# Kernel tuning notes

Measured on AMD Instinct MI355X. Metric: run time of the kernel, lower is better.

## Reference

```python
import jax, jax.numpy as jnp
import numpy as np

B, L, D = 1, 2048, 1024
H, F, HD = 16, 16, 64  # heads, feature_dim, head_dim
EPS = 1e-12


def setup_inputs() -> dict:
    key = jax.random.key(0)
    k1, k2, k3, k4, k5 = jax.random.split(key, 5)
    s = lambda fan_in: 1.0 / np.sqrt(fan_in)
    return {
        "hidden_states": jax.random.normal(k1, (B, L, D), jnp.float32),
        "Wq": jax.random.normal(k2, (D, H * F), jnp.float32) * s(D),
        "Wk": jax.random.normal(k3, (D, H * F), jnp.float32) * s(D),
        "Wv": jax.random.normal(k4, (D, H * HD), jnp.float32) * s(D),
        "Wo": jax.random.normal(k5, (H * HD, D), jnp.float32) * s(H * HD),
    }


def reference(hidden_states, Wq, Wk, Wv, Wo):
    b, l, _ = hidden_states.shape
    # projections (nn.Linear, no bias); reshape to (b, h, l, d)
    q = (hidden_states @ Wq).reshape(b, l, H, F).transpose(0, 2, 1, 3)
    k = (hidden_states @ Wk).reshape(b, l, H, F).transpose(0, 2, 1, 3)
    v = (hidden_states @ Wv).reshape(b, l, H, HD).transpose(0, 2, 1, 3)
    # feature map is identity. Causal quadratic linear attention:
    A = jnp.einsum("bhnd,bhmd->bhnm", q, k)          # [b,h,l,l]
    A = jnp.tril(A)
    y = jnp.einsum("bhnm,bhme->bhne", A, v)          # [b,h,l,hd]
    # denominator: q . cumsum(k)
    z = 1.0 / (jnp.einsum("bhld,bhld->bhl", q, jnp.cumsum(k, axis=2)) + EPS)
    y = y * z[..., None]
    # merge heads and output projection
    y = y.transpose(0, 2, 1, 3).reshape(b, l, H * HD)
    return y @ Wo
```

## Files before the change

### kernel.cpp

```cpp
#include <hip/hip_runtime.h>

constexpr int L  = 2048;
constexpr int D  = 1024;
constexpr int H  = 16;
constexpr int F  = 16;
constexpr int HD = 64;
constexpr int CHUNK = 128;
constexpr int NC = L / CHUNK;

typedef __bf16 bf16x8 __attribute__((ext_vector_type(8)));
typedef float  f32x16 __attribute__((ext_vector_type(16)));
typedef int    i32x4  __attribute__((ext_vector_type(4)));

__device__ __forceinline__ ushort f2bf(float f) {
  uint u = __builtin_bit_cast(uint, f);
  uint r = (u + 0x7FFFu + ((u >> 16) & 1u)) >> 16;
  return (ushort)r;
}

__device__ __forceinline__ void split5(float x, signed char s[5]) {
  float t = rintf(x * 16.f);              s[0] = (signed char)t;
  float r = fmaf(t, -6.25e-2f, x);
  t = rintf(r * 2048.f);                  s[1] = (signed char)t;
  r = fmaf(t, -4.8828125e-4f, r);
  t = rintf(r * 262144.f);                s[2] = (signed char)t;
  r = fmaf(t, -3.814697265625e-6f, r);
  t = rintf(r * 33554432.f);              s[3] = (signed char)t;
  r = fmaf(t, -2.9802322387695312e-8f, r);
  t = rintf(r * 4294967296.f);            s[4] = (signed char)t;
}

__global__ __launch_bounds__(256) void prep_all(
    const float* __restrict__ X,
    const float* __restrict__ Wv, const float* __restrict__ Wo,
    const float* __restrict__ Wq, const float* __restrict__ Wk,
    ushort* __restrict__ Ah, signed char* __restrict__ A8,
    ushort* __restrict__ BvT, ushort* __restrict__ BoT, signed char* __restrict__ W8) {
  __shared__ float t[32][33];
  const int tid = threadIdx.x;
  const int b = blockIdx.x;
  if (b < 2048) {
    const int plane = L * D;
    int idx = b * 256 + tid;
    float4 v = ((const float4*)X)[idx];
    ushort4 hh;
    hh.x = f2bf(v.x); hh.y = f2bf(v.y); hh.z = f2bf(v.z); hh.w = f2bf(v.w);
    ((ushort4*)Ah)[idx] = hh;
    signed char sx[5], sy[5], sz[5], sw[5];
    split5(v.x, sx); split5(v.y, sy); split5(v.z, sz); split5(v.w, sw);
    #pragma unroll
    for (int s = 0; s < 5; ++s) {
      char4 c; c.x = sx[s]; c.y = sy[s]; c.z = sz[s]; c.w = sw[s];
      ((char4*)(A8 + (size_t)s * plane))[idx] = c;
    }
    return;
  }
  const int bb = b - 2048;
  const int z = bb >> 10;
  const int bx = (bb & 1023) & 31, by = (bb & 1023) >> 5;
  const int lx = tid & 31, ly = tid >> 5;
  if (z == 2) {
    if (bx >= 16) return;
    const int plane = 512 * 1024;
    const int bn = bx * 32, bk = by * 32;
    const float* W = (bn < 256) ? Wq : Wk;
    const int wn = bn & 255;
    #pragma unroll
    for (int i = 0; i < 32; i += 8)
      t[ly + i][lx] = W[(size_t)(bk + ly + i) * 256 + wn + lx];
    __syncthreads();
    #pragma unroll
    for (int i = 0; i < 32; i += 8) {
      float v = t[lx][ly + i];
      signed char s[5];
      split5(v, s);
      size_t base = (size_t)(bn + ly + i) * 1024 + bk + lx;
      #pragma unroll
      for (int si = 0; si < 5; ++si) W8[(size_t)si * plane + base] = s[si];
    }
    return;
  }
  const float* W = z ? Wo : Wv;
  ushort* BT = z ? BoT : BvT;
  const int bn = bx * 32, bk = by * 32;
  #pragma unroll
  for (int i = 0; i < 32; i += 8)
    t[ly + i][lx] = W[(size_t)(bk + ly + i) * 1024 + bn + lx];
  __syncthreads();
  #pragma unroll
  for (int i = 0; i < 32; i += 8) {
    float v = t[lx][ly + i];
    BT[(size_t)(bn + ly + i) * 1024 + bk + lx] = f2bf(v);
  }
}

__global__ __launch_bounds__(512) void gemm_v_qk(
    const signed char* __restrict__ A8, const signed char* __restrict__ W8,
    float* __restrict__ Qo, float* __restrict__ Ko,
    const ushort* __restrict__ Av, const ushort* __restrict__ BvT,
    float* __restrict__ Vb) {
  __shared__ __align__(16) char lds_raw[51200];
  const int tid = threadIdx.x;
  const int bid = blockIdx.x;
  const int wave = tid >> 6, lane = tid & 63;

  if (bid < 256) {
    auto As = (signed char (*)[64][80])(lds_raw);
    auto Bs = (signed char (*)[64][80])(lds_raw + 25600);
    const int aplane = L * D;
    const int bplane = 512 * 1024;
    const int wm = (wave >> 2) * 32;
    const int wn = (wave & 3) * 16;
    int b2 = (bid & 7) * 32 + (bid >> 3);
    const int brow = (b2 >> 3) * 64, bcol = (b2 & 7) * 64;
    const int fr = lane & 15, kq = (lane >> 4) * 16;

    i32x4 acc[2][5];
    #pragma unroll
    for (int fm = 0; fm < 2; ++fm)
      #pragma unroll
      for (int g = 0; g < 5; ++g)
        #pragma unroll
        for (int r = 0; r < 4; ++r) acc[fm][g][r] = 0;

    for (int k0 = 0; k0 < D; k0 += 64) {
      #pragma unroll
      for (int i = 0; i < 5; ++i) {
        int c = i * 512 + tid;
        int side = (c >= 1280);
        int cc = side ? c - 1280 : c;
        int slice = cc >> 8, row = (cc & 255) >> 2, c16 = (cc & 3) * 16;
        const signed char* src = side
            ? &W8[(size_t)slice * bplane + (size_t)(bcol + row) * 1024 + k0 + c16]
            : &A8[(size_t)slice * aplane + (size_t)(brow + row) * 1024 + k0 + c16];
        int4 val = *(const int4*)src;
        signed char* dst = side ? &Bs[slice][row][c16] : &As[slice][row][c16];
        *(int4*)dst = val;
      }
      __syncthreads();
      i32x4 bfr[5], afr[2][5];
      #pragma unroll
      for (int s = 0; s < 5; ++s) bfr[s] = *(const i32x4*)&Bs[s][wn + fr][kq];
      #pragma unroll
      for (int fm = 0; fm < 2; ++fm)
        #pragma unroll
        for (int s = 0; s < 5; ++s)
          afr[fm][s] = *(const i32x4*)&As[s][wm + fm * 16 + fr][kq];
      #pragma unroll
      for (int fm = 0; fm < 2; ++fm) {
        acc[fm][0] = __builtin_amdgcn_mfma_i32_16x16x64_i8(afr[fm][0], bfr[0], acc[fm][0], 0, 0, 0);
        #pragma unroll
        for (int g = 1; g < 5; ++g)
          #pragma unroll
          for (int i = 0; i <= g; ++i)
            acc[fm][g] = __builtin_amdgcn_mfma_i32_16x16x64_i8(afr[fm][i], bfr[g - i], acc[fm][g], 0, 0, 0);
      }
      __syncthreads();
    }
    const double sc0 = 3.90625e-3, sc1 = 3.0517578125e-5, sc2 = 2.384185791015625e-7,
                 sc3 = 1.862645149230957e-9, sc4 = 1.4551915228366852e-11;
    float* Out = (bcol < 256) ? Qo : Ko;
    const int ocol = (bcol & 255) + wn + fr;
    #pragma unroll
    for (int fm = 0; fm < 2; ++fm)
      #pragma unroll
      for (int r = 0; r < 4; ++r) {
        double v = (double)acc[fm][0][r] * sc0 + (double)acc[fm][1][r] * sc1 +
                   (double)acc[fm][2][r] * sc2 + (double)acc[fm][3][r] * sc3 +
                   (double)acc[fm][4][r] * sc4;
        int row = brow + wm + fm * 16 + (lane >> 4) * 4 + r;
        Out[(size_t)row * 256 + ocol] = (float)v;
      }
    return;
  }

  auto AsV = (__bf16 (*)[128][40])(lds_raw);
  auto BsV = (__bf16 (*)[64][40])(lds_raw + 20480);
  const int vb0 = bid - 256;
  const int v2 = (vb0 & 7) * 32 + (vb0 >> 3);
  const int brow = (v2 >> 4) * 128, bcol = (v2 & 15) * 64;
  const int wm = (wave >> 1) * 32, wn = (wave & 1) * 32;
  const int srow = tid >> 2, skg = (tid & 3) * 8;
  const size_t a_off = (size_t)(brow + srow) * D + skg;
  const size_t b_off = (size_t)(bcol + (tid >> 2)) * D + skg;

  f32x16 acc;
  #pragma unroll
  for (int i = 0; i < 16; ++i) acc[i] = 0.f;

  bf16x8 ra, rb;
  auto LOADT = [&](int k0) {
    ra = *(const bf16x8*)&Av[a_off + k0];
    if (tid < 256) rb = *(const bf16x8*)&BvT[b_off + k0];
  };
  auto WRITET = [&](int buf) {
    *(bf16x8*)&AsV[buf][srow][skg] = ra;
    if (tid < 256) *(bf16x8*)&BsV[buf][tid >> 2][skg] = rb;
  };

  const int NS = D / 32;
  LOADT(0); WRITET(0);
  __syncthreads();
  int cur = 0;
  for (int t = 0; t < NS; ++t) {
    if (t + 1 < NS) LOADT((t + 1) * 32);
    const int fr = lane & 31;
    const int kh = (lane >> 5) * 8;
    bf16x8 a0 = *(const bf16x8*)&AsV[cur][wm + fr][kh];
    bf16x8 a1 = *(const bf16x8*)&AsV[cur][wm + fr][16 + kh];
    bf16x8 b0 = *(const bf16x8*)&BsV[cur][wn + fr][kh];
    bf16x8 b1 = *(const bf16x8*)&BsV[cur][wn + fr][16 + kh];
    acc = __builtin_amdgcn_mfma_f32_32x32x16_bf16(a0, b0, acc, 0, 0, 0);
    acc = __builtin_amdgcn_mfma_f32_32x32x16_bf16(a1, b1, acc, 0, 0, 0);
    if (t + 1 < NS) WRITET(cur ^ 1);
    __syncthreads();
    cur ^= 1;
  }
  const int fr = lane & 31, fq = lane >> 5;
  #pragma unroll
  for (int r = 0; r < 16; ++r) {
    int row = brow + wm + (r & 3) + 8 * (r >> 2) + 4 * fq;
    Vb[(size_t)row * 1024 + bcol + wn + fr] = acc[r];
  }
}

__global__ __launch_bounds__(256) void gemm_bf16_db(
    const ushort* __restrict__ A, const ushort* __restrict__ BT,
    float* __restrict__ C, int M, int N, int K) {
  constexpr int LDT = 40;
  __shared__ __bf16 As[2][64][LDT];
  __shared__ __bf16 Bs[2][64][LDT];
  const int tid  = threadIdx.x;
  const int wave = tid >> 6, lane = tid & 63;
  const int wr = (wave >> 1) * 32, wc = (wave & 1) * 32;
  const int nbx = gridDim.x, nwg = gridDim.x * gridDim.y;
  int bid = blockIdx.y * nbx + blockIdx.x;
  bid = (bid & 7) * (nwg >> 3) + (bid >> 3);
  const int brow = (bid / nbx) * 64, bcol = (bid % nbx) * 64;
  const int srow = tid >> 2, skg = (tid & 3) * 8;
  const size_t a_off = (size_t)(brow + srow) * K + skg;
  const size_t b_off = (size_t)(bcol + srow) * K + skg;

  f32x16 acc;
  #pragma unroll
  for (int i = 0; i < 16; ++i) acc[i] = 0.f;

  bf16x8 ra, rb;
  auto LOADT = [&](int k0) {
    ra = *(const bf16x8*)&A[a_off + k0];
    rb = *(const bf16x8*)&BT[b_off + k0];
  };
  auto WRITET = [&](int buf) {
    *(bf16x8*)&As[buf][srow][skg] = ra;
    *(bf16x8*)&Bs[buf][srow][skg] = rb;
  };

  const int NS = K / 32;
  LOADT(0); WRITET(0);
  __syncthreads();
  int cur = 0;
  for (int t = 0; t < NS; ++t) {
    if (t + 1 < NS) LOADT((t + 1) * 32);
    const int fr = lane & 31;
    const int kh = (lane >> 5) * 8;
    bf16x8 a0 = *(const bf16x8*)&As[cur][wr + fr][kh];
    bf16x8 a1 = *(const bf16x8*)&As[cur][wr + fr][16 + kh];
    bf16x8 b0 = *(const bf16x8*)&Bs[cur][wc + fr][kh];
    bf16x8 b1 = *(const bf16x8*)&Bs[cur][wc + fr][16 + kh];
    acc = __builtin_amdgcn_mfma_f32_32x32x16_bf16(a0, b0, acc, 0, 0, 0);
    acc = __builtin_amdgcn_mfma_f32_32x32x16_bf16(a1, b1, acc, 0, 0, 0);
    if (t + 1 < NS) WRITET(cur ^ 1);
    __syncthreads();
    cur ^= 1;
  }
  const int fr = lane & 31, fq = lane >> 5;
  #pragma unroll
  for (int r = 0; r < 16; ++r) {
    int row = brow + wr + (r & 3) + 8 * (r >> 2) + 4 * fq;
    C[(size_t)row * N + bcol + wc + fr] = acc[r];
  }
}

__global__ __launch_bounds__(256) void chunk_state(
    const float* __restrict__ Kq, const float* __restrict__ V,
    float* __restrict__ S, double* __restrict__ KS) {
  const int c = blockIdx.x, h = blockIdx.y;
  __shared__ float Ks[CHUNK][F];
  __shared__ float Vs[CHUNK][HD];
  const int tid = threadIdx.x;
  #pragma unroll
  for (int i = 0; i < 2; ++i) {
    int g = i * 256 + tid;
    int m = g >> 2, f0 = (g & 3) * 4;
    *(float4*)&Ks[m][f0] = *(const float4*)&Kq[(size_t)(c * CHUNK + m) * (H * F) + h * F + f0];
  }
  #pragma unroll
  for (int i = 0; i < 8; ++i) {
    int g = i * 256 + tid;
    int m = g >> 4, e0 = (g & 15) * 4;
    *(float4*)&Vs[m][e0] = *(const float4*)&V[(size_t)(c * CHUNK + m) * (H * HD) + h * HD + e0];
  }
  __syncthreads();
  const int f = tid >> 4, e0 = (tid & 15) * 4;
  float4 acc = make_float4(0.f, 0.f, 0.f, 0.f);
  for (int m = 0; m < CHUNK; ++m) {
    float kv = Ks[m][f];
    float4 v4 = *(const float4*)&Vs[m][e0];
    acc.x = fmaf(kv, v4.x, acc.x);
    acc.y = fmaf(kv, v4.y, acc.y);
    acc.z = fmaf(kv, v4.z, acc.z);
    acc.w = fmaf(kv, v4.w, acc.w);
  }
  *(float4*)&S[((((size_t)h * NC) + c) * F + f) * HD + e0] = acc;
  if (tid < F) {
    double s = 0.0;
    for (int m = 0; m < CHUNK; ++m) s += (double)Ks[m][tid];
    KS[(((size_t)h * NC) + c) * F + tid] = s;
  }
}

__global__ __launch_bounds__(512) void attn_chunk_v4(
    const float* __restrict__ Q, const float* __restrict__ Kq, const float* __restrict__ V,
    const float* __restrict__ S, const double* __restrict__ KS,
    ushort* __restrict__ Yh) {
  const int c = blockIdx.x, h = blockIdx.y;
  __shared__ float Ks[CHUNK][F];
  __shared__ float Vs[CHUNK][HD];
  __shared__ float Ss[F][HD];
  __shared__ double kcs[F];
  __shared__ float zs[CHUNK];
  const int tid = threadIdx.x;

  {
    int m = tid >> 2, f0 = (tid & 3) * 4;
    *(float4*)&Ks[m][f0] = *(const float4*)&Kq[(size_t)(c * CHUNK + m) * (H * F) + h * F + f0];
  }
  #pragma unroll
  for (int i = 0; i < 4; ++i) {
    int g = i * 512 + tid;
    int m = g >> 4, e0 = (g & 15) * 4;
    *(float4*)&Vs[m][e0] = *(const float4*)&V[(size_t)(c * CHUNK + m) * (H * HD) + h * HD + e0];
  }
  {
    float s0 = 0.f, s1 = 0.f;
    for (int cc = 0; cc < c; ++cc) {
      size_t base = (((size_t)h * NC) + cc) * (F * HD);
      s0 += S[base + tid];
      s1 += S[base + tid + 512];
    }
    ((float*)Ss)[tid] = s0;
    ((float*)Ss)[tid + 512] = s1;
  }
  if (tid < F) {
    double rk = 0.0;
    for (int cc = 0; cc < c; ++cc) rk += KS[(((size_t)h * NC) + cc) * F + tid];
    kcs[tid] = rk;
  }
  __syncthreads();

  const int w = tid >> 6;
  const int lane = tid & 63;
  const int rsub = lane >> 3;
  const int cg = lane & 7;
  const int e0 = cg * 8;
  const int lr = 8 * w + rsub;
  const int hr = 120 - 8 * w + rsub;

  float ql[F], qh[F];
  #pragma unroll
  for (int f0 = 0; f0 < F; f0 += 4) {
    *(float4*)&ql[f0] = *(const float4*)&Q[(size_t)(c * CHUNK + lr) * (H * F) + h * F + f0];
    *(float4*)&qh[f0] = *(const float4*)&Q[(size_t)(c * CHUNK + hr) * (H * F) + h * F + f0];
  }

  float accl[8], acch[8];
  #pragma unroll
  for (int j = 0; j < 8; ++j) { accl[j] = 0.f; acch[j] = 0.f; }
  float denl = 0.f, denh = 0.f;

  const int m1 = 8 * w + 8;
  const int m2 = 128 - 8 * w;
  for (int m = 0; m < m2; ++m) {
    float kr[F];
    #pragma unroll
    for (int f0 = 0; f0 < F; f0 += 4)
      *(float4*)&kr[f0] = *(const float4*)&Ks[m][f0];
    float v8[8];
    *(float4*)&v8[0] = *(const float4*)&Vs[m][e0];
    *(float4*)&v8[4] = *(const float4*)&Vs[m][e0 + 4];
    {
      float s = 0.f;
      #pragma unroll
      for (int f = 0; f < F; ++f) s = fmaf(qh[f], kr[f], s);
      float a = (m <= hr) ? s : 0.f;
      denh += a;
      #pragma unroll
      for (int j = 0; j < 8; ++j) acch[j] = fmaf(a, v8[j], acch[j]);
    }
    if (m < m1) {
      float s = 0.f;
      #pragma unroll
      for (int f = 0; f < F; ++f) s = fmaf(ql[f], kr[f], s);
      float a = (m <= lr) ? s : 0.f;
      denl += a;
      #pragma unroll
      for (int j = 0; j < 8; ++j) accl[j] = fmaf(a, v8[j], accl[j]);
    }
  }

  #pragma unroll
  for (int f = 0; f < F; ++f) {
    float s8[8];
    *(float4*)&s8[0] = *(const float4*)&Ss[f][e0];
    *(float4*)&s8[4] = *(const float4*)&Ss[f][e0 + 4];
    #pragma unroll
    for (int j = 0; j < 8; ++j) {
      accl[j] = fmaf(ql[f], s8[j], accl[j]);
      acch[j] = fmaf(qh[f], s8[j], acch[j]);
    }
  }

  if (cg == 0) {
    double dl = (double)denl, dh = (double)denh;
    #pragma unroll
    for (int f = 0; f < F; ++f) {
      dl += (double)ql[f] * kcs[f];
      dh += (double)qh[f] * kcs[f];
    }
    zs[lr] = (float)(1.0 / (dl + 1e-12));
    zs[hr] = (float)(1.0 / (dh + 1e-12));
  }
  __syncthreads();

  #pragma unroll
  for (int rr = 0; rr < 2; ++rr) {
    const int row = rr ? hr : lr;
    const float* ac = rr ? acch : accl;
    float zz = zs[row];
    ushort4 h4a, h4b;
    h4a.x = f2bf(ac[0] * zz); h4a.y = f2bf(ac[1] * zz);
    h4a.z = f2bf(ac[2] * zz); h4a.w = f2bf(ac[3] * zz);
    h4b.x = f2bf(ac[4] * zz); h4b.y = f2bf(ac[5] * zz);
    h4b.z = f2bf(ac[6] * zz); h4b.w = f2bf(ac[7] * zz);
    size_t base = (size_t)(c * CHUNK + row) * 1024 + h * HD + e0;
    *(ushort4*)&Yh[base]     = h4a;
    *(ushort4*)&Yh[base + 4] = h4b;
  }
}

extern "C" void kernel_launch(void* const* d_in, const int* in_sizes, int n_in,
                              void* d_out, int out_size, void* d_ws, size_t ws_size,
                              hipStream_t stream) {
  const float* hs = (const float*)d_in[0];
  const float* Wq = (const float*)d_in[1];
  const float* Wk = (const float*)d_in[2];
  const float* Wv = (const float*)d_in[3];
  const float* Wo = (const float*)d_in[4];
  float* out = (float*)d_out;

  char* ws = (char*)d_ws;
  const size_t MB = 1 << 20;
  signed char* A8 = (signed char*)(ws + 0 * MB);
  signed char* W8 = (signed char*)(ws + 10 * MB);
  ushort* Ah  = (ushort*)(ws + 13 * MB);
  ushort* BvT = (ushort*)(ws + 17 * MB);
  ushort* BoT = (ushort*)(ws + 19 * MB);
  float*  Vb  = (float*)(ws + 21 * MB);
  float*  Qb  = (float*)(ws + 29 * MB);
  float*  S   = (float*)(ws + 13 * MB);
  ushort* Ys  = (ushort*)(ws + 0 * MB);
  double* KS  = (double*)d_out;
  float*  Kb  = (float*)((char*)d_out + 1 * MB);

  prep_all<<<dim3(5120), 256, 0, stream>>>(hs, Wv, Wo, Wq, Wk, Ah, A8, BvT, BoT, W8);
  gemm_v_qk<<<dim3(512), 512, 0, stream>>>(A8, W8, Qb, Kb, Ah, BvT, Vb);
  chunk_state<<<dim3(NC, H), 256, 0, stream>>>(Kb, Vb, S, KS);
  attn_chunk_v4<<<dim3(NC, H), 512, 0, stream>>>(Qb, Kb, Vb, S, KS, Ys);
  gemm_bf16_db<<<dim3(16, 32), 256, 0, stream>>>(Ys, BoT, out, L, D, H * HD);
}
```

Baseline: 91.27 us.

## Fuse chunk-state into attention kernel and store V as bf16

Removes the separate chunk_state kernel: each attention block now recomputes the prefix K^T V state and K cumulative sums itself by looping over all earlier chunks and loading their K and V tiles. V is written by the projection GEMM in bf16 instead of fp32, which halves its memory traffic. Blocks are remapped with a swizzled 1D grid. The cost is redundant quadratic work across blocks: later chunks do up to 15 extra chunk-state passes, so block load becomes unbalanced. V also loses precision.

```diff
diff --git a/kernel.cpp b/kernel.cpp
--- a/kernel.cpp
+++ b/kernel.cpp
@@ -16,6 +16,10 @@
   uint u = __builtin_bit_cast(uint, f);
   uint r = (u + 0x7FFFu + ((u >> 16) & 1u)) >> 16;
   return (ushort)r;
+}
+__device__ __forceinline__ float bf2f(ushort h) {
+  uint u = ((uint)h) << 16;
+  return __builtin_bit_cast(float, u);
 }
 
 __device__ __forceinline__ void split5(float x, signed char s[5]) {
@@ -98,7 +102,7 @@
     const signed char* __restrict__ A8, const signed char* __restrict__ W8,
     float* __restrict__ Qo, float* __restrict__ Ko,
     const ushort* __restrict__ Av, const ushort* __restrict__ BvT,
-    float* __restrict__ Vb) {
+    ushort* __restrict__ Vb16) {
   __shared__ __align__(16) char lds_raw[51200];
   const int tid = threadIdx.x;
   const int bid = blockIdx.x;
@@ -220,7 +224,170 @@
   #pragma unroll
   for (int r = 0; r < 16; ++r) {
     int row = brow + wm + (r & 3) + 8 * (r >> 2) + 4 * fq;
-    Vb[(size_t)row * 1024 + bcol + wn + fr] = acc[r];
+    Vb16[(size_t)row * 1024 + bcol + wn + fr] = f2bf(acc[r]);
+  }
+}
+
+__global__ __launch_bounds__(512) void attn_chunk_v5(
+    const float* __restrict__ Q, const float* __restrict__ Kq,
+    const ushort* __restrict__ Vb16, ushort* __restrict__ Yh) {
+  const int swz = (blockIdx.x & 7) * 32 + (blockIdx.x >> 3);
+  const int h = swz >> 4, c = swz & 15;
+  __shared__ float Ks[CHUNK][F];
+  __shared__ float Vs[CHUNK][HD];
+  __shared__ float Kst[CHUNK][17];
+  __shared__ ushort Vst[CHUNK][HD];
+  __shared__ float Ssh[F][HD];
+  __shared__ double kred[F][32];
+  __shared__ double kcs[F];
+  __shared__ float zs[CHUNK];
+  const int tid = threadIdx.x;
+
+  {
+    int m = tid >> 2, f0 = (tid & 3) * 4;
+    *(float4*)&Ks[m][f0] = *(const float4*)&Kq[(size_t)(c * CHUNK + m) * (H * F) + h * F + f0];
+  }
+  #pragma unroll
+  for (int i = 0; i < 2; ++i) {
+    int g = i * 512 + tid;
+    int m = g >> 3, e0 = (g & 7) * 8;
+    bf16x8 vv = *(const bf16x8*)&Vb16[(size_t)(c * CHUNK + m) * 1024 + h * HD + e0];
+    #pragma unroll
+    for (int j = 0; j < 8; ++j) Vs[m][e0 + j] = bf2f(((ushort*)&vv)[j]);
+  }
+
+  const int fS = tid >> 6;
+  const int eS = tid & 63;
+  const int fK = tid >> 5;
+  const int mK = tid & 31;
+  float s0 = 0.f, s1 = 0.f;
+  double kcp = 0.0;
+  for (int cc = 0; cc < c; ++cc) {
+    __syncthreads();
+    {
+      int m = tid >> 2, f0 = (tid & 3) * 4;
+      float4 kv = *(const float4*)&Kq[(size_t)(cc * CHUNK + m) * (H * F) + h * F + f0];
+      Kst[m][f0 + 0] = kv.x; Kst[m][f0 + 1] = kv.y;
+      Kst[m][f0 + 2] = kv.z; Kst[m][f0 + 3] = kv.w;
+    }
+    #pragma unroll
+    for (int i = 0; i < 2; ++i) {
+      int g = i * 512 + tid;
+      int m = g >> 3, e0 = (g & 7) * 8;
+      *(bf16x8*)&Vst[m][e0] =
+          *(const bf16x8*)&Vb16[(size_t)(cc * CHUNK + m) * 1024 + h * HD + e0];
+    }
+    __syncthreads();
+    for (int m = 0; m < CHUNK; ++m) {
+      float kA = Kst[m][fS];
+      float kB = Kst[m][fS + 8];
+      float v = bf2f(Vst[m][eS]);
+      s0 = fmaf(kA, v, s0);
+      s1 = fmaf(kB, v, s1);
+    }
+    #pragma unroll
+    for (int mm = 0; mm < 4; ++mm)
+      kcp += (double)Kst[mm * 32 + mK][fK];
+  }
+  kred[fK][mK] = kcp;
+  Ssh[fS][eS] = s0;
+  Ssh[fS + 8][eS] = s1;
+  __syncthreads();
+  if (tid < F) {
+    double s = 0.0;
+    #pragma unroll
+    for (int j = 0; j < 32; ++j) s += kred[tid][j];
+    kcs[tid] = s;
+  }
+  __syncthreads();
+
+  const int w = tid >> 6;
+  const int lane = tid & 63;
+  const int rsub = lane >> 3;
+  const int cg = lane & 7;
+  const int e0 = cg * 8;
+  const int lr = 8 * w + rsub;
+  const int hr = 120 - 8 * w + rsub;
+
+  float ql[F], qh[F];
+  #pragma unroll
+  for (int f0 = 0; f0 < F; f0 += 4) {
+    *(float4*)&ql[f0] = *(const float4*)&Q[(size_t)(c * CHUNK + lr) * (H * F) + h * F + f0];
+    *(float4*)&qh[f0] = *(const float4*)&Q[(size_t)(c * CHUNK + hr) * (H * F) + h * F + f0];
+  }
+
+  float accl[8], acch[8];
+  #pragma unroll
+  for (int j = 0; j < 8; ++j) { accl[j] = 0.f; acch[j] = 0.f; }
+  float denl = 0.f, denh = 0.f;
+
+  const int m1 = 8 * w + 8;
+  const int m2 = 128 - 8 * w;
+  for (int m = 0; m < m2; ++m) {
+    float kr[F];
+    #pragma unroll
+    for (int f0 = 0; f0 < F; f0 += 4)
+      *(float4*)&kr[f0] = *(const float4*)&Ks[m][f0];
+    float v8[8];
+    *(float4*)&v8[0] = *(const float4*)&Vs[m][e0];
+    *(float4*)&v8[4] = *(const float4*)&Vs[m][e0 + 4];
+    {
+      float s = 0.f;
+      #pragma unroll
+      for (int f = 0; f < F; ++f) s = fmaf(qh[f], kr[f], s);
+      float a = (m <= hr) ? s : 0.f;
+      denh += a;
+      #pragma unroll
+      for (int j = 0; j < 8; ++j) acch[j] = fmaf(a, v8[j], acch[j]);
+    }
+    if (m < m1) {
+      float s = 0.f;
+      #pragma unroll
+      for (int f = 0; f < F; ++f) s = fmaf(ql[f], kr[f], s);
+      float a = (m <= lr) ? s : 0.f;
+      denl += a;
+      #pragma unroll
+      for (int j = 0; j < 8; ++j) accl[j] = fmaf(a, v8[j], accl[j]);
+    }
+  }
+
+  #pragma unroll
+  for (int f = 0; f < F; ++f) {
+    float s8[8];
+    *(float4*)&s8[0] = *(const float4*)&Ssh[f][e0];
+    *(float4*)&s8[4] = *(const float4*)&Ssh[f][e0 + 4];
+    #pragma unroll
+    for (int j = 0; j < 8; ++j) {
+      accl[j] = fmaf(ql[f], s8[j], accl[j]);
+      acch[j] = fmaf(qh[f], s8[j], acch[j]);
+    }
+  }
+
+  if (cg == 0) {
+    double dl = (double)denl, dh = (double)denh;
+    #pragma unroll
+    for (int f = 0; f < F; ++f) {
+      dl += (double)ql[f] * kcs[f];
+      dh += (double)qh[f] * kcs[f];
+    }
+    zs[lr] = (float)(1.0 / (dl + 1e-12));
+    zs[hr] = (float)(1.0 / (dh + 1e-12));
+  }
+  __syncthreads();
+
+  #pragma unroll
+  for (int rr = 0; rr < 2; ++rr) {
+    const int row = rr ? hr : lr;
+    const float* ac = rr ? acch : accl;
+    float zz = zs[row];
+    ushort4 h4a, h4b;
+    h4a.x = f2bf(ac[0] * zz); h4a.y = f2bf(ac[1] * zz);
+    h4a.z = f2bf(ac[2] * zz); h4a.w = f2bf(ac[3] * zz);
+    h4b.x = f2bf(ac[4] * zz); h4b.y = f2bf(ac[5] * zz);
+    h4b.z = f2bf(ac[6] * zz); h4b.w = f2bf(ac[7] * zz);
+    size_t base = (size_t)(c * CHUNK + row) * 1024 + h * HD + e0;
+    *(ushort4*)&Yh[base]     = h4a;
+    *(ushort4*)&Yh[base + 4] = h4b;
   }
 }
 
@@ -281,173 +448,6 @@
   }
 }
 
-__global__ __launch_bounds__(256) void chunk_state(
-    const float* __restrict__ Kq, const float* __restrict__ V,
-    float* __restrict__ S, double* __restrict__ KS) {
-  const int c = blockIdx.x, h = blockIdx.y;
-  __shared__ float Ks[CHUNK][F];
-  __shared__ float Vs[CHUNK][HD];
-  const int tid = threadIdx.x;
-  #pragma unroll
-  for (int i = 0; i < 2; ++i) {
-    int g = i * 256 + tid;
-    int m = g >> 2, f0 = (g & 3) * 4;
-    *(float4*)&Ks[m][f0] = *(const float4*)&Kq[(size_t)(c * CHUNK + m) * (H * F) + h * F + f0];
-  }
-  #pragma unroll
-  for (int i = 0; i < 8; ++i) {
-    int g = i * 256 + tid;
-    int m = g >> 4, e0 = (g & 15) * 4;
-    *(float4*)&Vs[m][e0] = *(const float4*)&V[(size_t)(c * CHUNK + m) * (H * HD) + h * HD + e0];
-  }
-  __syncthreads();
-  const int f = tid >> 4, e0 = (tid & 15) * 4;
-  float4 acc = make_float4(0.f, 0.f, 0.f, 0.f);
-  for (int m = 0; m < CHUNK; ++m) {
-    float kv = Ks[m][f];
-    float4 v4 = *(const float4*)&Vs[m][e0];
-    acc.x = fmaf(kv, v4.x, acc.x);
-    acc.y = fmaf(kv, v4.y, acc.y);
-    acc.z = fmaf(kv, v4.z, acc.z);
-    acc.w = fmaf(kv, v4.w, acc.w);
-  }
-  *(float4*)&S[((((size_t)h * NC) + c) * F + f) * HD + e0] = acc;
-  if (tid < F) {
-    double s = 0.0;
-    for (int m = 0; m < CHUNK; ++m) s += (double)Ks[m][tid];
-    KS[(((size_t)h * NC) + c) * F + tid] = s;
-  }
-}
-
-__global__ __launch_bounds__(512) void attn_chunk_v4(
-    const float* __restrict__ Q, const float* __restrict__ Kq, const float* __restrict__ V,
-    const float* __restrict__ S, const double* __restrict__ KS,
-    ushort* __restrict__ Yh) {
-  const int c = blockIdx.x, h = blockIdx.y;
-  __shared__ float Ks[CHUNK][F];
-  __shared__ float Vs[CHUNK][HD];
-  __shared__ float Ss[F][HD];
-  __shared__ double kcs[F];
-  __shared__ float zs[CHUNK];
-  const int tid = threadIdx.x;
-
-  {
-    int m = tid >> 2, f0 = (tid & 3) * 4;
-    *(float4*)&Ks[m][f0] = *(const float4*)&Kq[(size_t)(c * CHUNK + m) * (H * F) + h * F + f0];
-  }
-  #pragma unroll
-  for (int i = 0; i < 4; ++i) {
-    int g = i * 512 + tid;
-    int m = g >> 4, e0 = (g & 15) * 4;
-    *(float4*)&Vs[m][e0] = *(const float4*)&V[(size_t)(c * CHUNK + m) * (H * HD) + h * HD + e0];
-  }
-  {
-    float s0 = 0.f, s1 = 0.f;
-    for (int cc = 0; cc < c; ++cc) {
-      size_t base = (((size_t)h * NC) + cc) * (F * HD);
-      s0 += S[base + tid];
-      s1 += S[base + tid + 512];
-    }
-    ((float*)Ss)[tid] = s0;
-    ((float*)Ss)[tid + 512] = s1;
-  }
-  if (tid < F) {
-    double rk = 0.0;
-    for (int cc = 0; cc < c; ++cc) rk += KS[(((size_t)h * NC) + cc) * F + tid];
-    kcs[tid] = rk;
-  }
-  __syncthreads();
-
-  const int w = tid >> 6;
-  const int lane = tid & 63;
-  const int rsub = lane >> 3;
-  const int cg = lane & 7;
-  const int e0 = cg * 8;
-  const int lr = 8 * w + rsub;
-  const int hr = 120 - 8 * w + rsub;
-
-  float ql[F], qh[F];
-  #pragma unroll
-  for (int f0 = 0; f0 < F; f0 += 4) {
-    *(float4*)&ql[f0] = *(const float4*)&Q[(size_t)(c * CHUNK + lr) * (H * F) + h * F + f0];
-    *(float4*)&qh[f0] = *(const float4*)&Q[(size_t)(c * CHUNK + hr) * (H * F) + h * F + f0];
-  }
-
-  float accl[8], acch[8];
-  #pragma unroll
-  for (int j = 0; j < 8; ++j) { accl[j] = 0.f; acch[j] = 0.f; }
-  float denl = 0.f, denh = 0.f;
-
-  const int m1 = 8 * w + 8;
-  const int m2 = 128 - 8 * w;
-  for (int m = 0; m < m2; ++m) {
-    float kr[F];
-    #pragma unroll
-    for (int f0 = 0; f0 < F; f0 += 4)
-      *(float4*)&kr[f0] = *(const float4*)&Ks[m][f0];
-    float v8[8];
-    *(float4*)&v8[0] = *(const float4*)&Vs[m][e0];
-    *(float4*)&v8[4] = *(const float4*)&Vs[m][e0 + 4];
-    {
-      float s = 0.f;
-      #pragma unroll
-      for (int f = 0; f < F; ++f) s = fmaf(qh[f], kr[f], s);
-      float a = (m <= hr) ? s : 0.f;
-      denh += a;
-      #pragma unroll
-      for (int j = 0; j < 8; ++j) acch[j] = fmaf(a, v8[j], acch[j]);
-    }
-    if (m < m1) {
-      float s = 0.f;
-      #pragma unroll
-      for (int f = 0; f < F; ++f) s = fmaf(ql[f], kr[f], s);
-      float a = (m <= lr) ? s : 0.f;
-      denl += a;
-      #pragma unroll
-      for (int j = 0; j < 8; ++j) accl[j] = fmaf(a, v8[j], accl[j]);
-    }
-  }
-
-  #pragma unroll
-  for (int f = 0; f < F; ++f) {
-    float s8[8];
-    *(float4*)&s8[0] = *(const float4*)&Ss[f][e0];
-    *(float4*)&s8[4] = *(const float4*)&Ss[f][e0 + 4];
-    #pragma unroll
-    for (int j = 0; j < 8; ++j) {
-      accl[j] = fmaf(ql[f], s8[j], accl[j]);
-      acch[j] = fmaf(qh[f], s8[j], acch[j]);
-    }
-  }
-
-  if (cg == 0) {
-    double dl = (double)denl, dh = (double)denh;
-    #pragma unroll
-    for (int f = 0; f < F; ++f) {
-      dl += (double)ql[f] * kcs[f];
-      dh += (double)qh[f] * kcs[f];
-    }
-    zs[lr] = (float)(1.0 / (dl + 1e-12));
-    zs[hr] = (float)(1.0 / (dh + 1e-12));
-  }
-  __syncthreads();
-
-  #pragma unroll
-  for (int rr = 0; rr < 2; ++rr) {
-    const int row = rr ? hr : lr;
-    const float* ac = rr ? acch : accl;
-    float zz = zs[row];
-    ushort4 h4a, h4b;
-    h4a.x = f2bf(ac[0] * zz); h4a.y = f2bf(ac[1] * zz);
-    h4a.z = f2bf(ac[2] * zz); h4a.w = f2bf(ac[3] * zz);
-    h4b.x = f2bf(ac[4] * zz); h4b.y = f2bf(ac[5] * zz);
-    h4b.z = f2bf(ac[6] * zz); h4b.w = f2bf(ac[7] * zz);
-    size_t base = (size_t)(c * CHUNK + row) * 1024 + h * HD + e0;
-    *(ushort4*)&Yh[base]     = h4a;
-    *(ushort4*)&Yh[base + 4] = h4b;
-  }
-}
-
 extern "C" void kernel_launch(void* const* d_in, const int* in_sizes, int n_in,
                               void* d_out, int out_size, void* d_ws, size_t ws_size,
                               hipStream_t stream) {
@@ -462,19 +462,16 @@
   const size_t MB = 1 << 20;
   signed char* A8 = (signed char*)(ws + 0 * MB);
   signed char* W8 = (signed char*)(ws + 10 * MB);
-  ushort* Ah  = (ushort*)(ws + 13 * MB);
-  ushort* BvT = (ushort*)(ws + 17 * MB);
-  ushort* BoT = (ushort*)(ws + 19 * MB);
-  float*  Vb  = (float*)(ws + 21 * MB);
-  float*  Qb  = (float*)(ws + 29 * MB);
-  float*  S   = (float*)(ws + 13 * MB);
-  ushort* Ys  = (ushort*)(ws + 0 * MB);
-  double* KS  = (double*)d_out;
-  float*  Kb  = (float*)((char*)d_out + 1 * MB);
+  ushort* Ah   = (ushort*)(ws + 13 * MB);
+  ushort* BvT  = (ushort*)(ws + 17 * MB);
+  ushort* BoT  = (ushort*)(ws + 19 * MB);
+  ushort* Vb16 = (ushort*)(ws + 21 * MB);
+  float*  Qb   = (float*)(ws + 25 * MB);
+  ushort* Ys   = (ushort*)(ws + 0 * MB);
+  float*  Kb   = (float*)((char*)d_out + 1 * MB);
 
   prep_all<<<dim3(5120), 256, 0, stream>>>(hs, Wv, Wo, Wq, Wk, Ah, A8, BvT, BoT, W8);
-  gemm_v_qk<<<dim3(512), 512, 0, stream>>>(A8, W8, Qb, Kb, Ah, BvT, Vb);
-  chunk_state<<<dim3(NC, H), 256, 0, stream>>>(Kb, Vb, S, KS);
-  attn_chunk_v4<<<dim3(NC, H), 512, 0, stream>>>(Qb, Kb, Vb, S, KS, Ys);
+  gemm_v_qk<<<dim3(512), 512, 0, stream>>>(A8, W8, Qb, Kb, Ah, BvT, Vb16);
+  attn_chunk_v5<<<dim3(256), 512, 0, stream>>>(Qb, Kb, Vb16, Ys);
   gemm_bf16_db<<<dim3(16, 32), 256, 0, stream>>>(Ys, BoT, out, L, D, H * HD);
 }
```

New measurement: 133.2 us. +46.0%, slower.
